# Optimization experiments

Measured on AMD Instinct MI355X. Metric: run time of the kernel, lower is better.

Reference implementation:

```python
import jax, jax.numpy as jnp
import numpy as np

B, V, D, R, E, LQ, LV, H = 4, 20000, 64, 64, 200000, 2, 2, 4
LN_EPS = 1e-5


def _ln(x, g, b):
    mu = x.mean(-1, keepdims=True)
    var = ((x - mu) ** 2).mean(-1, keepdims=True)
    return (x - mu) * jax.lax.rsqrt(var + LN_EPS) * g + b


def _mlp2(x, w1, b1, w2, b2):
    # Linear -> ReLU -> Linear (dropout inactive at inference)
    return jnp.maximum(x @ w1.T + b1, 0.0) @ w2.T + b2


def _rspmm(edge_index, zrel, x):
    # generalized_rspmm: out[head] += relation[rel] * input[tail], unit edge weights.
    # zrel: (b, R', d), x: (b, V, d), edge_index: (E, 3) = (head, rel, tail)
    b, r, d = zrel.shape
    zz = jnp.transpose(zrel, (1, 0, 2)).reshape(r, b * d)   # 'b r d -> r (b d)'
    xx = jnp.transpose(x, (1, 0, 2)).reshape(V, b * d)      # 'b v d -> v (b d)'
    msg = zz[edge_index[:, 1]] * xx[edge_index[:, 2]]       # (E, b*d)
    out = jax.ops.segment_sum(msg, edge_index[:, 0], num_segments=V)
    return jnp.transpose(out.reshape(V, b, d), (1, 0, 2))


def _attn(q, k, v):
    # Kernelized (softmax-free) linear attention with normalized q, k.
    b, n, d = q.shape
    dh = d // H
    sp = lambda t: t.reshape(b, n, H, dh).transpose(0, 2, 1, 3)
    q, k, v = sp(q), sp(k), sp(v)
    nrm = lambda t: t / jnp.maximum(jnp.linalg.norm(t, axis=-1, keepdims=True), 1e-12)
    q, k = nrm(q), nrm(k)
    kvs = jnp.einsum('bhvd,bhvD->bhdD', k, v)
    num = jnp.einsum('bhvd,bhdD->bhvD', q, kvs) + v.sum(2, keepdims=True) + v * n
    den = jnp.einsum('bhvd,bhd->bhv', q, k.sum(2)) + 2.0 * n
    out = num / den[..., None]
    return out.transpose(0, 2, 1, 3).reshape(b, n, d)


def setup_inputs() -> dict:
    key = jax.random.key(0)
    ki = iter(jax.random.split(key, 64))
    nrm = lambda shape, s=0.05: jax.random.normal(next(ki), shape, jnp.float32) * s
    inp = dict(
        x=nrm((B, V, D), 1.0),
        z=nrm((B, D), 1.0),
        rev_z=nrm((B, D), 1.0),
        qk_noise=nrm((B, V, 1), 4.0),  # torch normal_(0, 4)
        fc_qk_z_w=nrm((R * D, D)), fc_qk_z_b=jnp.zeros((R * D,), jnp.float32),
        fc_qk_x_w1=nrm((D, D + 1)), fc_qk_x_b1=jnp.zeros((D,), jnp.float32),
        fc_qk_x_w2=nrm((D, D)), fc_qk_x_b2=jnp.zeros((D,), jnp.float32),
        fc_v_x_w1=nrm((D, 2 * D)), fc_v_x_b1=jnp.zeros((D,), jnp.float32),
        fc_v_x_w2=nrm((D, D)), fc_v_x_b2=jnp.zeros((D,), jnp.float32),
        fc_to_qk_w=nrm((2 * D, D)), fc_to_qk_b=jnp.zeros((2 * D,), jnp.float32),
        qk_w1=nrm((LQ, D, D)), qk_b1=jnp.zeros((LQ, D), jnp.float32),
        qk_w2=nrm((LQ, D, D)), qk_b2=jnp.zeros((LQ, D), jnp.float32),
        qk_alpha=nrm((LQ, D), 1.0),
        qk_ng=jnp.ones((LQ, D), jnp.float32), qk_nb=jnp.zeros((LQ, D), jnp.float32),
        v_fcz_w=nrm((LV, R * D, D)), v_fcz_b=jnp.zeros((LV, R * D), jnp.float32),
        v_w1=nrm((LV, D, D)), v_b1=jnp.zeros((LV, D), jnp.float32),
        v_w2=nrm((LV, D, D)), v_b2=jnp.zeros((LV, D), jnp.float32),
        v_beta=nrm((LV, D), 1.0),
        v_ng=jnp.ones((LV, D), jnp.float32), v_nb=jnp.zeros((LV, D), jnp.float32),
        ffn_w1=nrm((D, D)), ffn_b1=jnp.zeros((D,), jnp.float32),
        ffn_w2=nrm((D, D)), ffn_b2=jnp.zeros((D,), jnp.float32),
        attn_norm_g=jnp.ones((D,), jnp.float32), attn_norm_b=jnp.zeros((D,), jnp.float32),
        norm_g=jnp.ones((D,), jnp.float32), norm_b=jnp.zeros((D,), jnp.float32),
        h_index=jax.random.randint(next(ki), (B,), 0, V),
        edge_index=jnp.stack([
            jax.random.randint(next(ki), (E,), 0, V),
            jax.random.randint(next(ki), (E,), 0, R),
            jax.random.randint(next(ki), (E,), 0, V)], axis=1),
    )
    return inp


def reference(x, z, rev_z, qk_noise, fc_qk_z_w, fc_qk_z_b, fc_qk_x_w1, fc_qk_x_b1,
              fc_qk_x_w2, fc_qk_x_b2, fc_v_x_w1, fc_v_x_b1, fc_v_x_w2, fc_v_x_b2,
              fc_to_qk_w, fc_to_qk_b, qk_w1, qk_b1, qk_w2, qk_b2, qk_alpha, qk_ng, qk_nb,
              v_fcz_w, v_fcz_b, v_w1, v_b1, v_w2, v_b2, v_beta, v_ng, v_nb,
              ffn_w1, ffn_b1, ffn_w2, ffn_b2, attn_norm_g, attn_norm_b, norm_g, norm_b,
              h_index, edge_index):
    b = x.shape[0]
    # QK branch
    qk_z = (z @ fc_qk_z_w.T + fc_qk_z_b).reshape(b, R, D)
    qk_x = _mlp2(jnp.concatenate([x, qk_noise], -1), fc_qk_x_w1, fc_qk_x_b1, fc_qk_x_w2, fc_qk_x_b2)
    for i in range(LQ):
        xs = qk_x
        out = _rspmm(edge_index, qk_z, qk_x)
        qk_x = _ln(_mlp2(out + qk_alpha[i] * qk_x, qk_w1[i], qk_b1[i], qk_w2[i], qk_b2[i]),
                   qk_ng[i], qk_nb[i]) + xs
    # V branch: one-hot head-node indicator
    v0 = jnp.zeros((b, V, D), x.dtype).at[jnp.arange(b), h_index].set(1.0)
    v_x = _mlp2(jnp.concatenate([x, v0], -1), fc_v_x_w1, fc_v_x_b1, fc_v_x_w2, fc_v_x_b2)
    for i in range(LV):
        xs = v_x
        zr = (z @ v_fcz_w[i].T + v_fcz_b[i]).reshape(b, R, D)
        out = _rspmm(edge_index, zr, v_x)
        v_x = _ln(_mlp2(out + v_beta[i] * v_x, v_w1[i], v_b1[i], v_w2[i], v_b2[i]),
                  v_ng[i], v_nb[i]) + xs
    # Linear attention
    qk = qk_x @ fc_to_qk_w.T + fc_to_qk_b
    q, k = qk[..., :D], qk[..., D:]
    x = _ln(x + _attn(q, k, v_x), attn_norm_g, attn_norm_b)
    x = _ln(x + _mlp2(x, ffn_w1, ffn_b1, ffn_w2, ffn_b2), norm_g, norm_b)
    return x
```

## Files before the change

### kernel.cpp

```cpp
#include <hip/hip_runtime.h>
#include <hip/hip_bf16.h>

#define BDIM 4
#define VDIM 20000
#define DDIM 64
#define RDIM 64
#define EDIM 200000
#define BV (BDIM*VDIM)
#define LN_EPS 1e-5f
#define NBB 125
#define NTILE 1250
#define NDB 625
#define NRB (VDIM/8)
#define NSC ((EDIM+255)/256)

typedef __hip_bfloat16 bf16;
typedef __attribute__((ext_vector_type(8))) short short8v;
typedef __attribute__((ext_vector_type(4))) float floatx4;

__device__ __forceinline__ float ldf(const float* p, size_t i){ return p[i]; }
__device__ __forceinline__ float ldf(const bf16* p, size_t i){ return __bfloat162float(p[i]); }
__device__ __forceinline__ void stf(float* p, size_t i, float v){ p[i] = v; }
__device__ __forceinline__ void stf(bf16* p, size_t i, float v){ p[i] = __float2bfloat16(v); }

__device__ __forceinline__ unsigned short f2b(float f){
  unsigned u = __builtin_bit_cast(unsigned, f);
  u += 0x7fffu + ((u >> 16) & 1u);
  return (unsigned short)(u >> 16);
}
__device__ __forceinline__ float b2f(unsigned short h){
  unsigned u = ((unsigned)h) << 16;
  return __builtin_bit_cast(float, u);
}
__device__ __forceinline__ float4 ldf4(const float* p, size_t i){ return *(const float4*)(p+i); }
__device__ __forceinline__ float4 ldf4(const bf16* p, size_t i){
  ushort4 u = *(const ushort4*)(p+i);
  return make_float4(b2f(u.x), b2f(u.y), b2f(u.z), b2f(u.w));
}
__device__ __forceinline__ int swz(int r, int c){ return r*64 + (c ^ ((r & 7) << 3)); }

__device__ __forceinline__ float dot4(float4 a, float4 b){
  return a.x*b.x + a.y*b.y + a.z*b.z + a.w*b.w;
}

__device__ __forceinline__ void wsync(){
  __builtin_amdgcn_wave_barrier();
  __asm__ volatile("" ::: "memory");
}

__device__ __forceinline__ ushort4 packb(float4 v){
  ushort4 t; t.x = f2b(v.x); t.y = f2b(v.y); t.z = f2b(v.z); t.w = f2b(v.w); return t;
}

__global__ void fill_kernel(float* __restrict__ out, float v, int n){
  int t = blockIdx.x * 256 + threadIdx.x;
  if (t < n) out[t] = v;
}

__global__ void setup_kernel(const int* __restrict__ ei_raw, int* __restrict__ flag,
                             int* __restrict__ counts,
                             const float* __restrict__ z,
                             const float* __restrict__ qkzw, const float* __restrict__ qkzb,
                             const float* __restrict__ vfw,  const float* __restrict__ vfb,
                             float* __restrict__ qk_z, float* __restrict__ zr){
  int bid = blockIdx.x, tid = threadIdx.x;
  if (bid == 272){
    int nz = 0;
    for (int j = 2*tid + 1; j < 1024; j += 512) nz |= (ei_raw[j] != 0);
    nz = __any(nz);
    __shared__ int r[4];
    if ((tid & 63) == 0) r[tid >> 6] = nz;
    __syncthreads();
    if (tid == 0) flag[0] = (r[0] | r[1] | r[2] | r[3]) ? 0 : 1;
    return;
  }
  if (bid < 80){
    int i = bid*256 + tid;
    if (i < VDIM + 1) counts[i] = 0;
    return;
  }
  int idx = (bid - 80)*256 + tid;
  if (idx >= 49152) return;
  int which = idx >> 14;
  int r = idx & 16383;
  int b = r >> 12;
  int j = r & 4095;
  const float* wrow; float bias; float* outp;
  if (which == 0){ wrow = qkzw + (size_t)j*DDIM; bias = qkzb[j]; outp = qk_z; }
  else { int i = which - 1; wrow = vfw + (size_t)(i*4096 + j)*DDIM; bias = vfb[i*4096 + j]; outp = zr + i*16384; }
  const float4* zr4 = (const float4*)(z + (size_t)b*DDIM);
  const float4* wr4 = (const float4*)wrow;
  float acc = bias;
  #pragma unroll
  for (int i = 0; i < 16; i++) acc += dot4(zr4[i], wr4[i]);
  outp[r] = acc;
}

__global__ void prep_count_kernel(const int* __restrict__ ei_raw, const int* __restrict__ hi_raw,
                                  const int* __restrict__ flag,
                                  int* __restrict__ hi, int* __restrict__ counts){
  int is64 = flag[0];
  int e = blockIdx.x * 256 + threadIdx.x;
  if (e < EDIM){
    int dst = is64 ? ei_raw[6*e]   : ei_raw[3*e];
    int rel = is64 ? ei_raw[6*e+2] : ei_raw[3*e+1];
    int src = is64 ? ei_raw[6*e+4] : ei_raw[3*e+2];
    if ((unsigned)dst < VDIM && (unsigned)rel < RDIM && (unsigned)src < VDIM)
      atomicAdd(&counts[dst], 1);
  }
  if (e < BDIM) hi[e] = is64 ? hi_raw[2*e] : hi_raw[e];
}

__global__ void scan_kernel(const int* __restrict__ counts, int* __restrict__ row_ptr, int* __restrict__ cursor){
  __shared__ int wsum[4];
  int tid = threadIdx.x, lane = tid & 63, wid = tid >> 6;
  const int SEG = (VDIM + 255) / 256;
  int lo = tid * SEG;
  int hi = lo + SEG; if (hi > VDIM) hi = VDIM;
  int s = 0;
  for (int i = lo; i < hi; i++) s += counts[i];
  int x = s;
  #pragma unroll
  for (int o = 1; o < 64; o <<= 1){
    int t = __shfl_up(x, o, 64);
    if (lane >= o) x += t;
  }
  if (lane == 63) wsum[wid] = x;
  __syncthreads();
  int wo = 0;
  for (int w = 0; w < wid; w++) wo += wsum[w];
  int run = wo + x - s;
  for (int i = lo; i < hi; i++){
    row_ptr[i] = run; cursor[i] = run; run += counts[i];
  }
  if (tid == 255) row_ptr[VDIM] = run;
}

template<typename T>
__global__ __launch_bounds__(256) void scatter_init_kernel(
    const int* __restrict__ ei_raw, const int* __restrict__ flag,
    int* __restrict__ cursor, int2* __restrict__ pk,
    const float* __restrict__ x, const float* __restrict__ noise, const int* __restrict__ h_index,
    const float* __restrict__ qw1, const float* __restrict__ qb1,
    const float* __restrict__ qw2, const float* __restrict__ qb2,
    const float* __restrict__ vw1, const float* __restrict__ vb1,
    const float* __restrict__ vw2, const float* __restrict__ vb2,
    T* __restrict__ A, T* __restrict__ B){
  if (blockIdx.x < NSC){
    int is64 = flag[0];
    int e = blockIdx.x * 256 + threadIdx.x;
    if (e < EDIM){
      int dst = is64 ? ei_raw[6*e]   : ei_raw[3*e];
      int rel = is64 ? ei_raw[6*e+2] : ei_raw[3*e+1];
      int src = is64 ? ei_raw[6*e+4] : ei_raw[3*e+2];
      if ((unsigned)dst < VDIM && (unsigned)rel < RDIM && (unsigned)src < VDIM){
        int p = atomicAdd(&cursor[dst], 1);
        pk[p] = make_int2(rel, src);
      }
    }
    return;
  }
  __shared__ unsigned short Tl[4][2048];
  __shared__ unsigned short Hl[4][1024];
  __shared__ float Nl[4][32];
  int tid = threadIdx.x, lane = tid & 63, wid = tid >> 6;
  int lr = lane & 15, lg = lane >> 4;
  unsigned short* Tw = Tl[wid];
  unsigned short* Hw = Hl[wid];
  floatx4 zz = {0.f, 0.f, 0.f, 0.f};
  int t0 = (blockIdx.x - NSC)*2;
  #pragma unroll
  for (int tt = 0; tt < 2; tt++){
    int row0 = (t0 + tt)*64 + wid*16;
    #pragma unroll
    for (int it = 0; it < 4; it++){
      int rl = it*4 + lg;
      size_t gi = (size_t)(row0 + rl)*64 + 4*lr;
      float4 x4 = ldf4(x, gi);
      *(ushort4*)&Tw[tt*1024 + swz(rl, 4*lr)] = packb(x4);
      if (lr == 0) Nl[wid][tt*16 + rl] = noise[row0 + rl];
    }
  }
  wsync();
  short8v a0[2], a1[2];
  #pragma unroll
  for (int tt = 0; tt < 2; tt++){
    a0[tt] = *(const short8v*)&Tw[tt*1024 + swz(lr, lg*8)];
    a1[tt] = *(const short8v*)&Tw[tt*1024 + swz(lr, 32 + lg*8)];
  }
  {
    short8v w1f[4][2], w2f[4][2];
    float wnl[4], b1l[4], b2l[4];
    #pragma unroll
    for (int nt = 0; nt < 4; nt++){
      int col = lr + 16*nt;
      wnl[nt] = qw1[col*65 + 64];
      b1l[nt] = qb1[col]; b2l[nt] = qb2[col];
      #pragma unroll
      for (int ks = 0; ks < 2; ks++){
        const float* p1 = qw1 + col*65 + ks*32 + lg*8;
        const float* p2 = qw2 + col*64 + ks*32 + lg*8;
        short8v f, gg;
        #pragma unroll
        for (int j = 0; j < 8; j++){ f[j] = (short)f2b(p1[j]); gg[j] = (short)f2b(p2[j]); }
        w1f[nt][ks] = f; w2f[nt][ks] = gg;
      }
    }
    #pragma unroll
    for (int tt = 0; tt < 2; tt++){
      int row0 = (t0 + tt)*64 + wid*16;
      float nzq[4];
      #pragma unroll
      for (int q = 0; q < 4; q++) nzq[q] = Nl[wid][tt*16 + lg*4 + q];
      #pragma unroll
      for (int nt = 0; nt < 4; nt++){
        floatx4 acc = zz;
        acc = __builtin_amdgcn_mfma_f32_16x16x32_bf16(a0[tt], w1f[nt][0], acc, 0, 0, 0);
        acc = __builtin_amdgcn_mfma_f32_16x16x32_bf16(a1[tt], w1f[nt][1], acc, 0, 0, 0);
        #pragma unroll
        for (int q = 0; q < 4; q++)
          Hw[swz(lg*4 + q, lr + 16*nt)] = f2b(fmaxf(acc[q] + b1l[nt] + wnl[nt]*nzq[q], 0.f));
      }
      wsync();
      short8v h0 = *(const short8v*)&Hw[swz(lr, lg*8)];
      short8v h1 = *(const short8v*)&Hw[swz(lr, 32 + lg*8)];
      #pragma unroll
      for (int nt = 0; nt < 4; nt++){
        floatx4 acc = zz;
        acc = __builtin_amdgcn_mfma_f32_16x16x32_bf16(h0, w2f[nt][0], acc, 0, 0, 0);
        acc = __builtin_amdgcn_mfma_f32_16x16x32_bf16(h1, w2f[nt][1], acc, 0, 0, 0);
        #pragma unroll
        for (int q = 0; q < 4; q++){
          int rl = lg*4 + q, c = lr + 16*nt;
          stf(A, (size_t)(row0 + rl)*64 + c, acc[q] + b2l[nt]);
        }
      }
      wsync();
    }
  }
  {
    short8v w1f[4][2], w2f[4][2];
    float rsvl[4], b1l[4], b2l[4];
    #pragma unroll
    for (int nt = 0; nt < 4; nt++){
      int col = lr + 16*nt;
      b1l[nt] = vb1[col]; b2l[nt] = vb2[col];
      const float4* r4 = (const float4*)(vw1 + col*128 + 64);
      float rsv = 0.f;
      #pragma unroll
      for (int i = 0; i < 16; i++){ float4 t = r4[i]; rsv += t.x + t.y + t.z + t.w; }
      rsvl[nt] = rsv;
      #pragma unroll
      for (int ks = 0; ks < 2; ks++){
        const float* p1 = vw1 + col*128 + ks*32 + lg*8;
        const float* p2 = vw2 + col*64 + ks*32 + lg*8;
        short8v f, gg;
        #pragma unroll
        for (int j = 0; j < 8; j++){ f[j] = (short)f2b(p1[j]); gg[j] = (short)f2b(p2[j]); }
        w1f[nt][ks] = f; w2f[nt][ks] = gg;
      }
    }
    #pragma unroll
    for (int tt = 0; tt < 2; tt++){
      int row0 = (t0 + tt)*64 + wid*16;
      int b = row0 / VDIM;
      int vb = row0 - b*VDIM;
      int hv = h_index[b];
      bool cq[4];
      #pragma unroll
      for (int q = 0; q < 4; q++) cq[q] = (vb + lg*4 + q) == hv;
      #pragma unroll
      for (int nt = 0; nt < 4; nt++){
        floatx4 acc = zz;
        acc = __builtin_amdgcn_mfma_f32_16x16x32_bf16(a0[tt], w1f[nt][0], acc, 0, 0, 0);
        acc = __builtin_amdgcn_mfma_f32_16x16x32_bf16(a1[tt], w1f[nt][1], acc, 0, 0, 0);
        #pragma unroll
        for (int q = 0; q < 4; q++)
          Hw[swz(lg*4 + q, lr + 16*nt)] = f2b(fmaxf(acc[q] + b1l[nt] + (cq[q] ? rsvl[nt] : 0.f), 0.f));
      }
      wsync();
      short8v h0 = *(const short8v*)&Hw[swz(lr, lg*8)];
      short8v h1 = *(const short8v*)&Hw[swz(lr, 32 + lg*8)];
      #pragma unroll
      for (int nt = 0; nt < 4; nt++){
        floatx4 acc = zz;
        acc = __builtin_amdgcn_mfma_f32_16x16x32_bf16(h0, w2f[nt][0], acc, 0, 0, 0);
        acc = __builtin_amdgcn_mfma_f32_16x16x32_bf16(h1, w2f[nt][1], acc, 0, 0, 0);
        #pragma unroll
        for (int q = 0; q < 4; q++){
          int rl = lg*4 + q, c = lr + 16*nt;
          stf(B, (size_t)(row0 + rl)*64 + c, acc[q] + b2l[nt]);
        }
      }
      wsync();
    }
  }
}

template<typename T>
__global__ __launch_bounds__(256) void rspmm_dual(
    const int* __restrict__ row_ptr, const int2* __restrict__ pk,
    const float* __restrict__ zA, const float* __restrict__ zB,
    const T* __restrict__ XA, const T* __restrict__ XB,
    T* __restrict__ outA, T* __restrict__ outB){
  int bid = blockIdx.x;
  bool cb = bid >= NRB;
  int v0 = (cb ? bid - NRB : bid) * 8;
  const float* zrel = cb ? zB : zA;
  const T* X = cb ? XB : XA;
  T* out = cb ? outB : outA;
  int btch = threadIdx.x >> 6, d = threadIdx.x & 63;
  int rp[9];
  #pragma unroll
  for (int i = 0; i < 9; i++) rp[i] = row_ptr[v0 + i];
  const float* zb = zrel + btch*RDIM*DDIM + d;
  size_t xb = (size_t)btch*VDIM*64 + d;
  size_t ob = ((size_t)btch*VDIM + v0)*64 + d;
  #pragma unroll 1
  for (int vi = 0; vi < 8; vi++){
    int s = rp[vi], e = rp[vi+1];
    float a0 = 0.f, a1 = 0.f, a2 = 0.f, a3 = 0.f;
    int i = s;
    for (; i + 4 <= e; i += 4){
      int2 e0 = pk[i], e1 = pk[i+1], e2 = pk[i+2], e3 = pk[i+3];
      float x0 = ldf(X, xb + (size_t)e0.y*64);
      float x1 = ldf(X, xb + (size_t)e1.y*64);
      float x2 = ldf(X, xb + (size_t)e2.y*64);
      float x3 = ldf(X, xb + (size_t)e3.y*64);
      a0 += zb[(size_t)e0.x*64] * x0;
      a1 += zb[(size_t)e1.x*64] * x1;
      a2 += zb[(size_t)e2.x*64] * x2;
      a3 += zb[(size_t)e3.x*64] * x3;
    }
    for (; i < e; i++){
      int2 ed = pk[i];
      a0 += zb[(size_t)ed.x*64] * ldf(X, xb + (size_t)ed.y*64);
    }
    stf(out, ob + (size_t)vi*64, a0 + a1 + a2 + a3);
  }
}


template<typename T>
__global__ __launch_bounds__(256) void loop_dual_kernel(
    const T* __restrict__ OA, T* __restrict__ XA,
    const T* __restrict__ OB, T* __restrict__ XB,
    const float* __restrict__ alA, const float* __restrict__ w1A, const float* __restrict__ b1A,
    const float* __restrict__ w2A, const float* __restrict__ b2A,
    const float* __restrict__ ngA, const float* __restrict__ nbA,
    const float* __restrict__ alB, const float* __restrict__ w1B, const float* __restrict__ b1B,
    const float* __restrict__ w2B, const float* __restrict__ b2B,
    const float* __restrict__ ngB, const float* __restrict__ nbB){
  __shared__ unsigned short Tl[4][2048];
  __shared__ unsigned short Xl[4][2048];
  __shared__ unsigned short Hl[4][1024];
  int bid = blockIdx.x;
  bool cb = bid >= NDB;
  int pb = cb ? bid - NDB : bid;
  const T* O = cb ? OB : OA;
  T* X = cb ? XB : XA;
  const float* alpha = cb ? alB : alA;
  const float* w1 = cb ? w1B : w1A;
  const float* b1 = cb ? b1B : b1A;
  const float* w2 = cb ? w2B : w2A;
  const float* b2 = cb ? b2B : b2A;
  const float* ng = cb ? ngB : ngA;
  const float* nb = cb ? nbB : nbA;
  int tid = threadIdx.x, lane = tid & 63, wid = tid >> 6;
  int lr = lane & 15, lg = lane >> 4;
  short8v w1f[4][2], w2f[4][2];
  #pragma unroll
  for (int nt = 0; nt < 4; nt++){
    int col = lr + 16*nt;
    #pragma unroll
    for (int ks = 0; ks < 2; ks++){
      const float* p1 = w1 + col*64 + ks*32 + lg*8;
      const float* p2 = w2 + col*64 + ks*32 + lg*8;
      short8v f, g;
      #pragma unroll
      for (int j = 0; j < 8; j++){ f[j] = (short)f2b(p1[j]); g[j] = (short)f2b(p2[j]); }
      w1f[nt][ks] = f; w2f[nt][ks] = g;
    }
  }
  float4 al = ((const float4*)alpha)[lr];
  float b1l[4], b2l[4], ngl[4], nbl[4];
  #pragma unroll
  for (int nt = 0; nt < 4; nt++){
    int c = lr + 16*nt;
    b1l[nt] = b1[c]; b2l[nt] = b2[c]; ngl[nt] = ng[c]; nbl[nt] = nb[c];
  }
  unsigned short* Tw = Tl[wid];
  unsigned short* Xw = Xl[wid];
  unsigned short* Hw = Hl[wid];
  floatx4 zz = {0.f, 0.f, 0.f, 0.f};
  int t0 = pb*2;
  #pragma unroll
  for (int tt = 0; tt < 2; tt++){
    int row0 = (t0 + tt)*64 + wid*16;
    #pragma unroll
    for (int it = 0; it < 4; it++){
      int rl = it*4 + lg;
      size_t gi = (size_t)(row0 + rl)*64 + 4*lr;
      float4 xs4 = ldf4(X, gi);
      float4 ov4 = ldf4(O, gi);
      int si = tt*1024 + swz(rl, 4*lr);
      float4 tv;
      tv.x = ov4.x + al.x*xs4.x;
      tv.y = ov4.y + al.y*xs4.y;
      tv.z = ov4.z + al.z*xs4.z;
      tv.w = ov4.w + al.w*xs4.w;
      *(ushort4*)&Tw[si] = packb(tv);
      *(ushort4*)&Xw[si] = packb(xs4);
    }
  }
  wsync();
  #pragma unroll
  for (int tt = 0; tt < 2; tt++){
    int row0 = (t0 + tt)*64 + wid*16;
    short8v a0 = *(const short8v*)&Tw[tt*1024 + swz(lr, lg*8)];
    short8v a1 = *(const short8v*)&Tw[tt*1024 + swz(lr, 32 + lg*8)];
    #pragma unroll
    for (int nt = 0; nt < 4; nt++){
      floatx4 acc = zz;
      acc = __builtin_amdgcn_mfma_f32_16x16x32_bf16(a0, w1f[nt][0], acc, 0, 0, 0);
      acc = __builtin_amdgcn_mfma_f32_16x16x32_bf16(a1, w1f[nt][1], acc, 0, 0, 0);
      #pragma unroll
      for (int q = 0; q < 4; q++)
        Hw[swz(lg*4 + q, lr + 16*nt)] = f2b(fmaxf(acc[q] + b1l[nt], 0.f));
    }
    wsync();
    short8v h0 = *(const short8v*)&Hw[swz(lr, lg*8)];
    short8v h1 = *(const short8v*)&Hw[swz(lr, 32 + lg*8)];
    float y[4][4];
    float s[4] = {0.f,0.f,0.f,0.f}, ss[4] = {0.f,0.f,0.f,0.f};
    #pragma unroll
    for (int nt = 0; nt < 4; nt++){
      floatx4 acc = zz;
      acc = __builtin_amdgcn_mfma_f32_16x16x32_bf16(h0, w2f[nt][0], acc, 0, 0, 0);
      acc = __builtin_amdgcn_mfma_f32_16x16x32_bf16(h1, w2f[nt][1], acc, 0, 0, 0);
      #pragma unroll
      for (int q = 0; q < 4; q++){
        float v = acc[q] + b2l[nt];
        y[nt][q] = v; s[q] += v; ss[q] += v*v;
      }
    }
    #pragma unroll
    for (int o = 1; o < 16; o <<= 1){
      #pragma unroll
      for (int q = 0; q < 4; q++){
        s[q] += __shfl_xor(s[q], o, 64);
        ss[q] += __shfl_xor(ss[q], o, 64);
      }
    }
    float mu[4], rs[4];
    #pragma unroll
    for (int q = 0; q < 4; q++){
      mu[q] = s[q]*(1.f/64.f);
      float var = fmaxf(ss[q]*(1.f/64.f) - mu[q]*mu[q], 0.f);
      rs[q] = rsqrtf(var + LN_EPS);
    }
    #pragma unroll
    for (int nt = 0; nt < 4; nt++){
      #pragma unroll
      for (int q = 0; q < 4; q++){
        int rl = lg*4 + q, c = lr + 16*nt;
        float xs = b2f(Xw[tt*1024 + swz(rl, c)]);
        float v = (y[nt][q] - mu[q])*rs[q]*ngl[nt] + nbl[nt] + xs;
        stf(X, (size_t)(row0 + rl)*64 + c, v);
      }
    }
    wsync();
  }
}

template<typename T>
__global__ __launch_bounds__(256) void kvred_mfma_kernel(
    const T* __restrict__ Xqk, const T* __restrict__ Xv,
    const float* __restrict__ w, const float* __restrict__ bias,
    float* __restrict__ partial){
  __shared__ unsigned short T1[4][1024];
  __shared__ unsigned short T2[4][1024];
  __shared__ float red[4*1536];
  int tid = threadIdx.x, lane = tid & 63, wid = tid >> 6;
  int lr = lane & 15, lg = lane >> 4;
  short8v wkf[4][2];
  #pragma unroll
  for (int nt = 0; nt < 4; nt++){
    int col = 64 + lr + 16*nt;
    #pragma unroll
    for (int ks = 0; ks < 2; ks++){
      const float* p = w + col*64 + ks*32 + lg*8;
      short8v f;
      #pragma unroll
      for (int j = 0; j < 8; j++) f[j] = (short)f2b(p[j]);
      wkf[nt][ks] = f;
    }
  }
  float bk[4];
  #pragma unroll
  for (int nt = 0; nt < 4; nt++) bk[nt] = bias[64 + lr + 16*nt];
  int b = blockIdx.x / NBB, blk = blockIdx.x % NBB;
  unsigned short* Tw = T1[wid];
  unsigned short* Vw = T2[wid];
  floatx4 zz = {0.f, 0.f, 0.f, 0.f};
  floatx4 kvacc[4] = {zz, zz, zz, zz};
  float ksp[4] = {0.f,0.f,0.f,0.f};
  float vsp[4] = {0.f,0.f,0.f,0.f};
  const short8v z8 = {0,0,0,0,0,0,0,0};
  for (int st = blk*4 + wid; st < 1250; st += NBB*4){
    size_t gr = (size_t)b*VDIM + (size_t)st*16;
    #pragma unroll
    for (int it = 0; it < 4; it++){
      int rl = it*4 + lg;
      size_t gi = (gr + rl)*64 + 4*lr;
      float4 xq4 = ldf4(Xqk, gi);
      float4 xv4 = ldf4(Xv, gi);
      int si = swz(rl, 4*lr);
      *(ushort4*)&Tw[si] = packb(xq4);
      *(ushort4*)&Vw[si] = packb(xv4);
      vsp[0] += xv4.x; vsp[1] += xv4.y; vsp[2] += xv4.z; vsp[3] += xv4.w;
    }
    wsync();
    short8v a0 = *(const short8v*)&Tw[swz(lr, lg*8)];
    short8v a1 = *(const short8v*)&Tw[swz(lr, 32 + lg*8)];
    float kn[4][4];
    #pragma unroll
    for (int nt = 0; nt < 4; nt++){
      floatx4 acc = zz;
      acc = __builtin_amdgcn_mfma_f32_16x16x32_bf16(a0, wkf[nt][0], acc, 0, 0, 0);
      acc = __builtin_amdgcn_mfma_f32_16x16x32_bf16(a1, wkf[nt][1], acc, 0, 0, 0);
      #pragma unroll
      for (int q = 0; q < 4; q++) kn[nt][q] = acc[q] + bk[nt];
    }
    #pragma unroll
    for (int nt = 0; nt < 4; nt++){
      float n0 = kn[nt][0]*kn[nt][0], n1 = kn[nt][1]*kn[nt][1];
      float n2 = kn[nt][2]*kn[nt][2], n3 = kn[nt][3]*kn[nt][3];
      #pragma unroll
      for (int o = 1; o < 16; o <<= 1){
        n0 += __shfl_xor(n0, o, 64); n1 += __shfl_xor(n1, o, 64);
        n2 += __shfl_xor(n2, o, 64); n3 += __shfl_xor(n3, o, 64);
      }
      kn[nt][0] /= fmaxf(sqrtf(n0), 1e-12f);
      kn[nt][1] /= fmaxf(sqrtf(n1), 1e-12f);
      kn[nt][2] /= fmaxf(sqrtf(n2), 1e-12f);
      kn[nt][3] /= fmaxf(sqrtf(n3), 1e-12f);
      ksp[nt] += kn[nt][0] + kn[nt][1] + kn[nt][2] + kn[nt][3];
    }
    wsync();
    #pragma unroll
    for (int nt = 0; nt < 4; nt++){
      int c = lr + 16*nt;
      #pragma unroll
      for (int q = 0; q < 4; q++)
        Tw[c*16 + lg*4 + q] = f2b(kn[nt][q]);
    }
    wsync();
    #pragma unroll
    for (int nt = 0; nt < 4; nt++){
      short8v af = z8, bf = z8;
      if (lg < 2){
        af = *(const short8v*)&Tw[(nt*16 + lr)*16 + lg*8];
        #pragma unroll
        for (int j = 0; j < 8; j++)
          bf[j] = (short)Vw[swz(lg*8 + j, nt*16 + lr)];
      }
      kvacc[nt] = __builtin_amdgcn_mfma_f32_16x16x32_bf16(af, bf, kvacc[nt], 0, 0, 0);
    }
    wsync();
  }
  float* rw = red + wid*1536;
  #pragma unroll
  for (int nt = 0; nt < 4; nt++){
    #pragma unroll
    for (int q = 0; q < 4; q++)
      rw[(nt*16 + lg*4 + q)*16 + lr] = kvacc[nt][q];
    rw[1024 + lg*64 + lr + 16*nt] = ksp[nt];
  }
  #pragma unroll
  for (int m = 0; m < 4; m++)
    rw[1280 + lg*64 + 4*lr + m] = vsp[m];
  __syncthreads();
  float* P = partial + (size_t)blockIdx.x*1152;
  for (int j = tid; j < 1152; j += 256){
    float s = 0.f;
    if (j < 1024){
      #pragma unroll
      for (int wv = 0; wv < 4; wv++) s += red[wv*1536 + j];
    } else if (j < 1088){
      int c = j - 1024;
      #pragma unroll
      for (int wv = 0; wv < 4; wv++)
        #pragma unroll
        for (int gg = 0; gg < 4; gg++) s += red[wv*1536 + 1024 + gg*64 + c];
    } else {
      int c = j - 1088;
      #pragma unroll
      for (int wv = 0; wv < 4; wv++)
        #pragma unroll
        for (int gg = 0; gg < 4; gg++) s += red[wv*1536 + 1280 + gg*64 + c];
    }
    P[j] = s;
  }
}

__global__ void qkred_kernel(const float* __restrict__ partial,
                             float* __restrict__ kvs, float* __restrict__ ksum, float* __restrict__ vsum,
                             unsigned short* __restrict__ kvsb, unsigned short* __restrict__ ksb){
  int b = blockIdx.x / 5, ch = blockIdx.x % 5;
  int j = ch*256 + threadIdx.x;
  if (j >= 1152) return;
  const float* P = partial + (size_t)b*NBB*1152;
  float s = 0.f;
  for (int t = 0; t < NBB; t++) s += P[(size_t)t*1152 + j];
  if (j < 1024){      kvs[b*1024 + j] = s; kvsb[b*1024 + j] = f2b(s); }
  else if (j < 1088){ ksum[b*64 + (j-1024)] = s; ksb[b*64 + (j-1024)] = f2b(s); }
  else                vsum[b*64 + (j-1088)] = s;
}

template<typename T>
__global__ __launch_bounds__(256) void attn_final_kernel(
    const float* __restrict__ x, const T* __restrict__ A, const T* __restrict__ Xv,
    const unsigned short* __restrict__ kvsb, const unsigned short* __restrict__ ksb,
    const float* __restrict__ vsum,
    const float* __restrict__ w, const float* __restrict__ bias,
    const float* __restrict__ ag, const float* __restrict__ ab,
    const float* __restrict__ fw1, const float* __restrict__ fb1,
    const float* __restrict__ fw2, const float* __restrict__ fb2,
    const float* __restrict__ g, const float* __restrict__ bb,
    float* __restrict__ out){
  __shared__ unsigned short Ql[4][2048];
  __shared__ unsigned short Hl[4][1024];
  int tid = threadIdx.x, lane = tid & 63, wid = tid >> 6;
  int lr = lane & 15, lg = lane >> 4;
  short8v wqf[4][2];
  #pragma unroll
  for (int nt = 0; nt < 4; nt++){
    int col = lr + 16*nt;
    #pragma unroll
    for (int ks = 0; ks < 2; ks++){
      const float* p = w + col*64 + ks*32 + lg*8;
      short8v f;
      #pragma unroll
      for (int j = 0; j < 8; j++) f[j] = (short)f2b(p[j]);
      wqf[nt][ks] = f;
    }
  }
  short8v f1f[4][2], f2f[4][2];
  float bq[4], agl[4], abl[4], b1l[4], b2l[4], gl[4], bl[4];
  #pragma unroll
  for (int nt = 0; nt < 4; nt++){
    int col = lr + 16*nt;
    bq[nt] = bias[col]; agl[nt] = ag[col]; abl[nt] = ab[col];
    b1l[nt] = fb1[col]; b2l[nt] = fb2[col]; gl[nt] = g[col]; bl[nt] = bb[col];
    #pragma unroll
    for (int ks = 0; ks < 2; ks++){
      const float* p1 = fw1 + col*64 + ks*32 + lg*8;
      const float* p2 = fw2 + col*64 + ks*32 + lg*8;
      short8v f, gg;
      #pragma unroll
      for (int j = 0; j < 8; j++){ f[j] = (short)f2b(p1[j]); gg[j] = (short)f2b(p2[j]); }
      f1f[nt][ks] = f; f2f[nt][ks] = gg;
    }
  }
  unsigned short* Qw = Ql[wid];
  unsigned short* Hw = Hl[wid];
  floatx4 zz = {0.f, 0.f, 0.f, 0.f};
  const short8v z8 = {0,0,0,0,0,0,0,0};
  int t0 = blockIdx.x*2;
  #pragma unroll
  for (int tt = 0; tt < 2; tt++){
    int row0 = (t0 + tt)*64 + wid*16;
    #pragma unroll
    for (int it = 0; it < 4; it++){
      int rl = it*4 + lg;
      size_t gi = (size_t)(row0 + rl)*64 + 4*lr;
      *(ushort4*)&Qw[tt*1024 + swz(rl, 4*lr)] = packb(ldf4(A, gi));
    }
  }
  wsync();
  #pragma unroll
  for (int tt = 0; tt < 2; tt++){
    int row0 = (t0 + tt)*64 + wid*16;
    int b = row0 / VDIM;
    short8v a0 = *(const short8v*)&Qw[tt*1024 + swz(lr, lg*8)];
    short8v a1 = *(const short8v*)&Qw[tt*1024 + swz(lr, 32 + lg*8)];
    float qn[4][4];
    #pragma unroll
    for (int nt = 0; nt < 4; nt++){
      floatx4 acc = zz;
      acc = __builtin_amdgcn_mfma_f32_16x16x32_bf16(a0, wqf[nt][0], acc, 0, 0, 0);
      acc = __builtin_amdgcn_mfma_f32_16x16x32_bf16(a1, wqf[nt][1], acc, 0, 0, 0);
      #pragma unroll
      for (int q = 0; q < 4; q++) qn[nt][q] = acc[q] + bq[nt];
    }
    #pragma unroll
    for (int nt = 0; nt < 4; nt++){
      float n0 = qn[nt][0]*qn[nt][0], n1 = qn[nt][1]*qn[nt][1];
      float n2 = qn[nt][2]*qn[nt][2], n3 = qn[nt][3]*qn[nt][3];
      #pragma unroll
      for (int o = 1; o < 16; o <<= 1){
        n0 += __shfl_xor(n0, o, 64); n1 += __shfl_xor(n1, o, 64);
        n2 += __shfl_xor(n2, o, 64); n3 += __shfl_xor(n3, o, 64);
      }
      qn[nt][0] /= fmaxf(sqrtf(n0), 1e-12f);
      qn[nt][1] /= fmaxf(sqrtf(n1), 1e-12f);
      qn[nt][2] /= fmaxf(sqrtf(n2), 1e-12f);
      qn[nt][3] /= fmaxf(sqrtf(n3), 1e-12f);
    }
    wsync();
    #pragma unroll
    for (int nt = 0; nt < 4; nt++){
      #pragma unroll
      for (int q = 0; q < 4; q++)
        Qw[tt*1024 + swz(lg*4 + q, lr + 16*nt)] = f2b(qn[nt][q]);
    }
    wsync();
    float y[4][4];
    float s[4] = {0.f,0.f,0.f,0.f}, ss[4] = {0.f,0.f,0.f,0.f};
    #pragma unroll
    for (int nt = 0; nt < 4; nt++){
      short8v af = z8, bn = z8, bd = z8;
      if (lg < 2){
        af = *(const short8v*)&Qw[tt*1024 + swz(lr, nt*16 + lg*8)];
        bd = *(const short8v*)&ksb[b*64 + nt*16 + lg*8];
        #pragma unroll
        for (int j = 0; j < 8; j++)
          bn[j] = (short)kvsb[b*1024 + (nt*16 + lg*8 + j)*16 + lr];
      }
      int c = lr + 16*nt;
      float vsb = vsum[b*64 + c];
      floatx4 numc, denc;
      #pragma unroll
      for (int q = 0; q < 4; q++){
        float vv = ldf(Xv, (size_t)(row0 + lg*4 + q)*64 + c);
        numc[q] = vsb + vv*(float)VDIM;
        denc[q] = 2.0f*(float)VDIM;
      }
      numc = __builtin_amdgcn_mfma_f32_16x16x32_bf16(af, bn, numc, 0, 0, 0);
      denc = __builtin_amdgcn_mfma_f32_16x16x32_bf16(af, bd, denc, 0, 0, 0);
      #pragma unroll
      for (int q = 0; q < 4; q++){
        float xv = x[(size_t)(row0 + lg*4 + q)*64 + c];
        float v = xv + numc[q]/denc[q];
        y[nt][q] = v; s[q] += v; ss[q] += v*v;
      }
    }
    #pragma unroll
    for (int o = 1; o < 16; o <<= 1){
      #pragma unroll
      for (int q = 0; q < 4; q++){
        s[q] += __shfl_xor(s[q], o, 64);
        ss[q] += __shfl_xor(ss[q], o, 64);
      }
    }
    #pragma unroll
    for (int q = 0; q < 4; q++){
      float mu = s[q]*(1.f/64.f);
      float var = fmaxf(ss[q]*(1.f/64.f) - mu*mu, 0.f);
      float rs = rsqrtf(var + LN_EPS);
      #pragma unroll
      for (int nt = 0; nt < 4; nt++)
        y[nt][q] = (y[nt][q] - mu)*rs*agl[nt] + abl[nt];
    }
    wsync();
    #pragma unroll
    for (int nt = 0; nt < 4; nt++){
      #pragma unroll
      for (int q = 0; q < 4; q++)
        Qw[tt*1024 + swz(lg*4 + q, lr + 16*nt)] = f2b(y[nt][q]);
    }
    wsync();
    short8v xa0 = *(const short8v*)&Qw[tt*1024 + swz(lr, lg*8)];
    short8v xa1 = *(const short8v*)&Qw[tt*1024 + swz(lr, 32 + lg*8)];
    #pragma unroll
    for (int nt = 0; nt < 4; nt++){
      floatx4 acc = zz;
      acc = __builtin_amdgcn_mfma_f32_16x16x32_bf16(xa0, f1f[nt][0], acc, 0, 0, 0);
      acc = __builtin_amdgcn_mfma_f32_16x16x32_bf16(xa1, f1f[nt][1], acc, 0, 0, 0);
      #pragma unroll
      for (int q = 0; q < 4; q++)
        Hw[swz(lg*4 + q, lr + 16*nt)] = f2b(fmaxf(acc[q] + b1l[nt], 0.f));
    }
    wsync();
    short8v h0 = *(const short8v*)&Hw[swz(lr, lg*8)];
    short8v h1 = *(const short8v*)&Hw[swz(lr, 32 + lg*8)];
    float t[4][4];
    float s2[4] = {0.f,0.f,0.f,0.f}, ss2[4] = {0.f,0.f,0.f,0.f};
    #pragma unroll
    for (int nt = 0; nt < 4; nt++){
      floatx4 acc = zz;
      acc = __builtin_amdgcn_mfma_f32_16x16x32_bf16(h0, f2f[nt][0], acc, 0, 0, 0);
      acc = __builtin_amdgcn_mfma_f32_16x16x32_bf16(h1, f2f[nt][1], acc, 0, 0, 0);
      #pragma unroll
      for (int q = 0; q < 4; q++){
        float v = acc[q] + b2l[nt] + y[nt][q];
        t[nt][q] = v; s2[q] += v; ss2[q] += v*v;
      }
    }
    #pragma unroll
    for (int o = 1; o < 16; o <<= 1){
      #pragma unroll
      for (int q = 0; q < 4; q++){
        s2[q] += __shfl_xor(s2[q], o, 64);
        ss2[q] += __shfl_xor(ss2[q], o, 64);
      }
    }
    #pragma unroll
    for (int q = 0; q < 4; q++){
      float mu = s2[q]*(1.f/64.f);
      float var = fmaxf(ss2[q]*(1.f/64.f) - mu*mu, 0.f);
      float rs = rsqrtf(var + LN_EPS);
      #pragma unroll
      for (int nt = 0; nt < 4; nt++){
        int c = lr + 16*nt;
        out[(size_t)(row0 + lg*4 + q)*64 + c] = (t[nt][q] - mu)*rs*gl[nt] + bl[nt];
      }
    }
    wsync();
  }
}

static const int DICT_SIZES[42] = {
  5120000,256,256,80000,262144,4096,4160,64,4096,64,
  8192,64,4096,64,8192,128,8192,128,8192,128,
  128,128,128,524288,8192,8192,128,8192,128,128,
  128,128,4096,64,4096,64,64,64,64,64,
  4,600000};

template<typename T>
static void run_pipeline(const float* const* N, const int* hi,
                         const int* ei_raw, const int* eflag,
                         int* cursor, int2* pk, const int* row_ptr,
                         float* qk_z, float* zr, float* kvs, float* part,
                         unsigned short* kvsb,
                         T* A, T* B, T* OA, T* OB, bool dual,
                         float* outp, hipStream_t stream){
  float* ksum = kvs + 4096;
  float* vsum = kvs + 4352;
  unsigned short* ksb = kvsb + 4096;

  scatter_init_kernel<T><<<NSC + NDB, 256, 0, stream>>>(ei_raw, eflag, cursor, pk,
      N[0], N[3], hi, N[6], N[7], N[8], N[9], N[10], N[11], N[12], N[13], A, B);

  if (dual){
    for (int i = 0; i < 2; i++){
      rspmm_dual<T><<<2*NRB, 256, 0, stream>>>(row_ptr, pk, qk_z, zr + i*16384, A, B, OA, OB);
      loop_dual_kernel<T><<<2*NDB, 256, 0, stream>>>(OA, A, OB, B,
          N[20] + i*64, N[16] + i*4096, N[17] + i*64, N[18] + i*4096, N[19] + i*64, N[21] + i*64, N[22] + i*64,
          N[29] + i*64, N[25] + i*4096, N[26] + i*64, N[27] + i*4096, N[28] + i*64, N[30] + i*64, N[31] + i*64);
    }
  } else {
    for (int i = 0; i < 2; i++){
      rspmm_dual<T><<<NRB, 256, 0, stream>>>(row_ptr, pk, qk_z, qk_z, A, A, OA, OA);
      loop_dual_kernel<T><<<NDB, 256, 0, stream>>>(OA, A, OA, A,
          N[20] + i*64, N[16] + i*4096, N[17] + i*64, N[18] + i*4096, N[19] + i*64, N[21] + i*64, N[22] + i*64,
          N[20] + i*64, N[16] + i*4096, N[17] + i*64, N[18] + i*4096, N[19] + i*64, N[21] + i*64, N[22] + i*64);
    }
    for (int i = 0; i < 2; i++){
      rspmm_dual<T><<<NRB, 256, 0, stream>>>(row_ptr, pk, zr + i*16384, zr + i*16384, B, B, OA, OA);
      loop_dual_kernel<T><<<NDB, 256, 0, stream>>>(OA, B, OA, B,
          N[29] + i*64, N[25] + i*4096, N[26] + i*64, N[27] + i*4096, N[28] + i*64, N[30] + i*64, N[31] + i*64,
          N[29] + i*64, N[25] + i*4096, N[26] + i*64, N[27] + i*4096, N[28] + i*64, N[30] + i*64, N[31] + i*64);
    }
  }

  kvred_mfma_kernel<T><<<BDIM*NBB, 256, 0, stream>>>(A, B, N[14], N[15], part);
  qkred_kernel<<<20, 256, 0, stream>>>(part, kvs, ksum, vsum, kvsb, ksb);
  attn_final_kernel<T><<<NDB, 256, 0, stream>>>(N[0], A, B, kvsb, ksb, vsum,
      N[14], N[15], N[36], N[37], N[32], N[33], N[34], N[35], N[38], N[39], outp);
}

extern "C" void kernel_launch(void* const* d_in, const int* in_sizes, int n_in,
                              void* d_out, int out_size, void* d_ws, size_t ws_size,
                              hipStream_t stream){
  float* outp = (float*)d_out;
  const int GOUT = (out_size + 255) / 256;

  if (n_in != 42){
    fill_kernel<<<GOUT, 256, 0, stream>>>(outp, 2000.0f + (float)n_in, out_size);
    return;
  }
  auto sz_ok = [&](int s, int e)->bool{
    if (s == e) return true;
    if ((e == 4 || e == 600000) && s == 2*e) return true;
    return false;
  };
  int bad = -1;
  for (int i = 0; i < 42 && bad < 0; i++)
    if (!sz_ok(in_sizes[i], DICT_SIZES[i])) bad = i;
  if (bad >= 0){
    fill_kernel<<<GOUT, 256, 0, stream>>>(outp, 1000.0f + (float)bad, out_size);
    return;
  }

  const float* N[40];
  for (int i = 0; i < 40; i++) N[i] = (const float*)d_in[i];
  const int* hi_raw = (const int*)d_in[40];
  const int* ei_raw = (const int*)d_in[41];

  char* p = (char*)d_ws;
  auto alloc = [&](size_t bytes)->char*{ char* r = p; p += (bytes + 255) / 256 * 256; return r; };
  int* hi      = (int*)alloc(256);
  int* eflag   = (int*)alloc(256);
  int* counts  = (int*)alloc((VDIM+1)*4);
  int* row_ptr = (int*)alloc((VDIM+1)*4);
  int* cursor  = (int*)alloc((VDIM+1)*4);
  int2* pk     = (int2*)alloc((size_t)EDIM*8);
  float* qk_z  = (float*)alloc(16384u*4);
  float* zr    = (float*)alloc(32768u*4);
  float* kvs   = (float*)alloc(4608u*4);
  unsigned short* kvsb = (unsigned short*)alloc(4352u*2);
  float* part  = (float*)alloc((size_t)BDIM*NBB*1152*4);
  size_t fixed = (size_t)(p - (char*)d_ws);
  const size_t bufH = (size_t)BV*64*2;

  setup_kernel<<<273, 256, 0, stream>>>(ei_raw, eflag, counts,
      N[1], N[4], N[5], N[23], N[24], qk_z, zr);
  prep_count_kernel<<<(EDIM+255)/256, 256, 0, stream>>>(ei_raw, hi_raw, eflag, hi, counts);
  scan_kernel<<<1, 256, 0, stream>>>(counts, row_ptr, cursor);

  if (ws_size >= fixed + 4*bufH + 1024){
    bf16* A  = (bf16*)alloc(bufH);
    bf16* B  = (bf16*)alloc(bufH);
    bf16* OA = (bf16*)alloc(bufH);
    bf16* OB = (bf16*)alloc(bufH);
    run_pipeline<bf16>(N, hi, ei_raw, eflag, cursor, pk, row_ptr,
                       qk_z, zr, kvs, part, kvsb, A, B, OA, OB, true, outp, stream);
  } else {
    bf16* A  = (bf16*)alloc(bufH);
    bf16* B  = (bf16*)alloc(bufH);
    bf16* OA = (bf16*)alloc(bufH);
    run_pipeline<bf16>(N, hi, ei_raw, eflag, cursor, pk, row_ptr,
                       qk_z, zr, kvs, part, kvsb, A, B, OA, OA, false, outp, stream);
  }
}
```

Baseline: 531.4 us.

## Move query projection and normalization into extra blocks of the KV-reduction kernel

The q projection (MFMA with the fc_to_qk weights plus bias) and per-head L2 normalization move out of attn_final_kernel into extra blocks of the KV-reduction kernel. Those blocks write normalized q to a scratch buffer, and attn_final now just loads it into shared memory. The aim is to shorten the serial attention-output kernel, cut its register pressure and a pair of wave syncs, and let the q work overlap with the KV reduction. In exchange it adds a full write and read of the q tensor through global memory. The raw ushort4 load assumes the element type T is bf16.

New measurement: 517.7 us. 2.6% less time.

```diff
diff --git a/kernel.cpp b/kernel.cpp
--- a/kernel.cpp
+++ b/kernel.cpp
@@ -13,6 +13,7 @@
 #define NDB 625
 #define NRB (VDIM/8)
 #define NSC ((EDIM+255)/256)
+#define NKV (BDIM*NBB)
 
 typedef __hip_bfloat16 bf16;
 typedef __attribute__((ext_vector_type(8))) short short8v;
@@ -474,15 +475,77 @@
 }
 
 template<typename T>
-__global__ __launch_bounds__(256) void kvred_mfma_kernel(
+__global__ __launch_bounds__(256) void kvred_qproj_kernel(
     const T* __restrict__ Xqk, const T* __restrict__ Xv,
     const float* __restrict__ w, const float* __restrict__ bias,
-    float* __restrict__ partial){
+    float* __restrict__ partial, T* __restrict__ qn_out){
   __shared__ unsigned short T1[4][1024];
   __shared__ unsigned short T2[4][1024];
   __shared__ float red[4*1536];
   int tid = threadIdx.x, lane = tid & 63, wid = tid >> 6;
   int lr = lane & 15, lg = lane >> 4;
+  floatx4 zz = {0.f, 0.f, 0.f, 0.f};
+  const short8v z8 = {0,0,0,0,0,0,0,0};
+
+  if (blockIdx.x >= NKV){
+    int tile = blockIdx.x - NKV;
+    unsigned short* Tw = T1[wid];
+    short8v wqf[4][2];
+    float bq[4];
+    #pragma unroll
+    for (int nt = 0; nt < 4; nt++){
+      int col = lr + 16*nt;
+      bq[nt] = bias[col];
+      #pragma unroll
+      for (int ks = 0; ks < 2; ks++){
+        const float* p = w + col*64 + ks*32 + lg*8;
+        short8v f;
+        #pragma unroll
+        for (int j = 0; j < 8; j++) f[j] = (short)f2b(p[j]);
+        wqf[nt][ks] = f;
+      }
+    }
+    int row0 = tile*64 + wid*16;
+    #pragma unroll
+    for (int it = 0; it < 4; it++){
+      int rl = it*4 + lg;
+      size_t gi = (size_t)(row0 + rl)*64 + 4*lr;
+      *(ushort4*)&Tw[swz(rl, 4*lr)] = packb(ldf4(Xqk, gi));
+    }
+    wsync();
+    short8v a0 = *(const short8v*)&Tw[swz(lr, lg*8)];
+    short8v a1 = *(const short8v*)&Tw[swz(lr, 32 + lg*8)];
+    float qn[4][4];
+    #pragma unroll
+    for (int nt = 0; nt < 4; nt++){
+      floatx4 acc = zz;
+      acc = __builtin_amdgcn_mfma_f32_16x16x32_bf16(a0, wqf[nt][0], acc, 0, 0, 0);
+      acc = __builtin_amdgcn_mfma_f32_16x16x32_bf16(a1, wqf[nt][1], acc, 0, 0, 0);
+      #pragma unroll
+      for (int q = 0; q < 4; q++) qn[nt][q] = acc[q] + bq[nt];
+    }
+    #pragma unroll
+    for (int nt = 0; nt < 4; nt++){
+      float n0 = qn[nt][0]*qn[nt][0], n1 = qn[nt][1]*qn[nt][1];
+      float n2 = qn[nt][2]*qn[nt][2], n3 = qn[nt][3]*qn[nt][3];
+      #pragma unroll
+      for (int o = 1; o < 16; o <<= 1){
+        n0 += __shfl_xor(n0, o, 64); n1 += __shfl_xor(n1, o, 64);
+        n2 += __shfl_xor(n2, o, 64); n3 += __shfl_xor(n3, o, 64);
+      }
+      qn[nt][0] /= fmaxf(sqrtf(n0), 1e-12f);
+      qn[nt][1] /= fmaxf(sqrtf(n1), 1e-12f);
+      qn[nt][2] /= fmaxf(sqrtf(n2), 1e-12f);
+      qn[nt][3] /= fmaxf(sqrtf(n3), 1e-12f);
+    }
+    #pragma unroll
+    for (int nt = 0; nt < 4; nt++)
+      #pragma unroll
+      for (int q = 0; q < 4; q++)
+        stf(qn_out, (size_t)(row0 + lg*4 + q)*64 + lr + 16*nt, qn[nt][q]);
+    return;
+  }
+
   short8v wkf[4][2];
   #pragma unroll
   for (int nt = 0; nt < 4; nt++){
@@ -502,11 +565,9 @@
   int b = blockIdx.x / NBB, blk = blockIdx.x % NBB;
   unsigned short* Tw = T1[wid];
   unsigned short* Vw = T2[wid];
-  floatx4 zz = {0.f, 0.f, 0.f, 0.f};
   floatx4 kvacc[4] = {zz, zz, zz, zz};
   float ksp[4] = {0.f,0.f,0.f,0.f};
   float vsp[4] = {0.f,0.f,0.f,0.f};
-  const short8v z8 = {0,0,0,0,0,0,0,0};
   for (int st = blk*4 + wid; st < 1250; st += NBB*4){
     size_t gr = (size_t)b*VDIM + (size_t)st*16;
     #pragma unroll
@@ -620,10 +681,9 @@
 
 template<typename T>
 __global__ __launch_bounds__(256) void attn_final_kernel(
-    const float* __restrict__ x, const T* __restrict__ A, const T* __restrict__ Xv,
+    const float* __restrict__ x, const T* __restrict__ QN, const T* __restrict__ Xv,
     const unsigned short* __restrict__ kvsb, const unsigned short* __restrict__ ksb,
     const float* __restrict__ vsum,
-    const float* __restrict__ w, const float* __restrict__ bias,
     const float* __restrict__ ag, const float* __restrict__ ab,
     const float* __restrict__ fw1, const float* __restrict__ fb1,
     const float* __restrict__ fw2, const float* __restrict__ fb2,
@@ -633,25 +693,12 @@
   __shared__ unsigned short Hl[4][1024];
   int tid = threadIdx.x, lane = tid & 63, wid = tid >> 6;
   int lr = lane & 15, lg = lane >> 4;
-  short8v wqf[4][2];
+  short8v f1f[4][2], f2f[4][2];
+  float agl[4], abl[4], b1l[4], b2l[4], gl[4], bl[4];
   #pragma unroll
   for (int nt = 0; nt < 4; nt++){
     int col = lr + 16*nt;
-    #pragma unroll
-    for (int ks = 0; ks < 2; ks++){
-      const float* p = w + col*64 + ks*32 + lg*8;
-      short8v f;
-      #pragma unroll
-      for (int j = 0; j < 8; j++) f[j] = (short)f2b(p[j]);
-      wqf[nt][ks] = f;
-    }
-  }
-  short8v f1f[4][2], f2f[4][2];
-  float bq[4], agl[4], abl[4], b1l[4], b2l[4], gl[4], bl[4];
-  #pragma unroll
-  for (int nt = 0; nt < 4; nt++){
-    int col = lr + 16*nt;
-    bq[nt] = bias[col]; agl[nt] = ag[col]; abl[nt] = ab[col];
+    agl[nt] = ag[col]; abl[nt] = ab[col];
     b1l[nt] = fb1[col]; b2l[nt] = fb2[col]; gl[nt] = g[col]; bl[nt] = bb[col];
     #pragma unroll
     for (int ks = 0; ks < 2; ks++){
@@ -675,7 +722,7 @@
     for (int it = 0; it < 4; it++){
       int rl = it*4 + lg;
       size_t gi = (size_t)(row0 + rl)*64 + 4*lr;
-      *(ushort4*)&Qw[tt*1024 + swz(rl, 4*lr)] = packb(ldf4(A, gi));
+      *(ushort4*)&Qw[tt*1024 + swz(rl, 4*lr)] = *(const ushort4*)&QN[gi];
     }
   }
   wsync();
@@ -683,39 +730,6 @@
   for (int tt = 0; tt < 2; tt++){
     int row0 = (t0 + tt)*64 + wid*16;
     int b = row0 / VDIM;
-    short8v a0 = *(const short8v*)&Qw[tt*1024 + swz(lr, lg*8)];
-    short8v a1 = *(const short8v*)&Qw[tt*1024 + swz(lr, 32 + lg*8)];
-    float qn[4][4];
-    #pragma unroll
-    for (int nt = 0; nt < 4; nt++){
-      floatx4 acc = zz;
-      acc = __builtin_amdgcn_mfma_f32_16x16x32_bf16(a0, wqf[nt][0], acc, 0, 0, 0);
-      acc = __builtin_amdgcn_mfma_f32_16x16x32_bf16(a1, wqf[nt][1], acc, 0, 0, 0);
-      #pragma unroll
-      for (int q = 0; q < 4; q++) qn[nt][q] = acc[q] + bq[nt];
-    }
-    #pragma unroll
-    for (int nt = 0; nt < 4; nt++){
-      float n0 = qn[nt][0]*qn[nt][0], n1 = qn[nt][1]*qn[nt][1];
-      float n2 = qn[nt][2]*qn[nt][2], n3 = qn[nt][3]*qn[nt][3];
-      #pragma unroll
-      for (int o = 1; o < 16; o <<= 1){
-        n0 += __shfl_xor(n0, o, 64); n1 += __shfl_xor(n1, o, 64);
-        n2 += __shfl_xor(n2, o, 64); n3 += __shfl_xor(n3, o, 64);
-      }
-      qn[nt][0] /= fmaxf(sqrtf(n0), 1e-12f);
-      qn[nt][1] /= fmaxf(sqrtf(n1), 1e-12f);
-      qn[nt][2] /= fmaxf(sqrtf(n2), 1e-12f);
-      qn[nt][3] /= fmaxf(sqrtf(n3), 1e-12f);
-    }
-    wsync();
-    #pragma unroll
-    for (int nt = 0; nt < 4; nt++){
-      #pragma unroll
-      for (int q = 0; q < 4; q++)
-        Qw[tt*1024 + swz(lg*4 + q, lr + 16*nt)] = f2b(qn[nt][q]);
-    }
-    wsync();
     float y[4][4];
     float s[4] = {0.f,0.f,0.f,0.f}, ss[4] = {0.f,0.f,0.f,0.f};
     #pragma unroll
@@ -865,10 +879,10 @@
     }
   }
 
-  kvred_mfma_kernel<T><<<BDIM*NBB, 256, 0, stream>>>(A, B, N[14], N[15], part);
+  kvred_qproj_kernel<T><<<NKV + NTILE, 256, 0, stream>>>(A, B, N[14], N[15], part, OA);
   qkred_kernel<<<20, 256, 0, stream>>>(part, kvs, ksum, vsum, kvsb, ksb);
-  attn_final_kernel<T><<<NDB, 256, 0, stream>>>(N[0], A, B, kvsb, ksb, vsum,
-      N[14], N[15], N[36], N[37], N[32], N[33], N[34], N[35], N[38], N[39], outp);
+  attn_final_kernel<T><<<NDB, 256, 0, stream>>>(N[0], OA, B, kvsb, ksb, vsum,
+      N[36], N[37], N[32], N[33], N[34], N[35], N[38], N[39], outp);
 }
 
 extern "C" void kernel_launch(void* const* d_in, const int* in_sizes, int n_in,
```
